# Kernel tuning notes

Hardware: AMD Instinct MI355X
Metric: run time of the kernel (lower is better)

## Reference

```python
import jax, jax.numpy as jnp
import numpy as np

N_NODES = 50000
N_EDGES = 800000
IN_F = 64
OUT_F = 64
HEADS = 4
ALPHA = 0.2  # LeakyReLU negative slope


def setup_inputs() -> dict:
    key = jax.random.key(0)
    k1, k2, k3, k4, k5, k6 = jax.random.split(key, 6)
    x = jax.random.normal(k1, (N_NODES, IN_F), dtype=jnp.float32)
    src = jax.random.randint(k2, (N_EDGES,), 0, N_NODES)
    dst = jax.random.randint(k3, (N_EDGES,), 0, N_NODES)
    edge_index = jnp.stack([src, dst]).astype(jnp.int64)
    # learned params: per-head projection + attention vectors (GAT)
    W = jax.random.normal(k4, (HEADS, IN_F, OUT_F), dtype=jnp.float32) * 0.1
    a_src = jax.random.normal(k5, (HEADS, OUT_F), dtype=jnp.float32) * 0.1
    a_dst = jax.random.normal(k6, (HEADS, OUT_F), dtype=jnp.float32) * 0.1
    return {"x": x, "edge_index": edge_index, "W": W, "a_src": a_src, "a_dst": a_dst}


def reference(x, edge_index, W, a_src, a_dst):
    N = x.shape[0]
    src, dst = edge_index[0], edge_index[1]
    # per-head projection: [N, H, O]
    h = jnp.einsum('nf,hfo->nho', x, W)
    # node-level attention halves: [N, H]
    s_src = jnp.einsum('nho,ho->nh', h, a_src)
    s_dst = jnp.einsum('nho,ho->nh', h, a_dst)
    # edge logits with LeakyReLU: [E, H]
    e = jax.nn.leaky_relu(s_src[src] + s_dst[dst], negative_slope=ALPHA)
    # segment softmax over incoming edges of each destination node
    e_max = jax.ops.segment_max(e, dst, num_segments=N)  # [N, H]
    e_exp = jnp.exp(e - e_max[dst])
    denom = jax.ops.segment_sum(e_exp, dst, num_segments=N)  # [N, H]
    attn = e_exp / (denom[dst] + 1e-16)  # [E, H]
    # weighted scatter-aggregation: [N, H, O]
    msg = h[src] * attn[:, :, None]
    out = jax.ops.segment_sum(msg, dst, num_segments=N)
    # average_head=False -> concatenate heads; no bias, no activation
    return out.reshape(N, HEADS * OUT_F)
```

## Files before the change

kernel.cpp:

```cpp
#include <hip/hip_runtime.h>

#define HEADS 4
#define OUTF 64
#define INF 64
#define CAP 48

typedef __attribute__((ext_vector_type(8))) short bf16x8;
typedef __attribute__((ext_vector_type(4))) float f32x4;

__device__ __forceinline__ ushort f2bf(float f) {
    const unsigned u = __float_as_uint(f);
    return (ushort)((u + 0x7fffu + ((u >> 16) & 1u)) >> 16);
}

__global__ __launch_bounds__(256) void prep_kernel(
    const float* __restrict__ W, const float* __restrict__ a_src,
    const float* __restrict__ a_dst, float* __restrict__ va_s, float* __restrict__ va_d,
    ushort* __restrict__ W_packed, const int* __restrict__ ei, int* __restrict__ flag,
    int* __restrict__ deg, int N)
{
    const int t = threadIdx.x;
    for (int i = blockIdx.x * 256 + t; i < N; i += gridDim.x * 256) deg[i] = 0;

    if (blockIdx.x == 8) {
        if (t == 0) {
            int all0 = 1;
            #pragma unroll
            for (int k = 1; k < 64; k += 2) all0 &= (ei[k] == 0);
            *flag = all0;
        }
        const int h = t >> 6;
        const float* Wr = W + (size_t)t * 64;
        const float* as = a_src + h * 64;
        const float* ad = a_dst + h * 64;
        float s = 0.f, d = 0.f;
        #pragma unroll
        for (int o = 0; o < 64; ++o) {
            const float wv = Wr[o];
            s = fmaf(wv, as[o], s);
            d = fmaf(wv, ad[o], d);
        }
        va_s[t] = s;
        va_d[t] = d;
        return;
    }
    const int idx  = blockIdx.x * 256 + t;
    const int tile = idx >> 7;
    const int st   = (idx >> 6) & 1;
    const int l    = idx & 63;
    const int o_g  = tile * 16 + (l & 15);
    const int hh   = o_g >> 6;
    const int oo   = o_g & 63;
    const int k0   = st * 32 + (l >> 4) * 8;
    ushort v[8];
    #pragma unroll
    for (int i = 0; i < 8; ++i)
        v[i] = f2bf(W[(size_t)hh * 4096 + (size_t)(k0 + i) * 64 + oo]);
    uint4 u;
    u.x = v[0] | ((unsigned)v[1] << 16);
    u.y = v[2] | ((unsigned)v[3] << 16);
    u.z = v[4] | ((unsigned)v[5] << 16);
    u.w = v[6] | ((unsigned)v[7] << 16);
    *reinterpret_cast<uint4*>(W_packed + (size_t)idx * 8) = u;
}

__global__ __launch_bounds__(256) void s_fill_kernel(
    const float* __restrict__ x, const float* __restrict__ va_s,
    const float* __restrict__ va_d, float* __restrict__ ssrc,
    float* __restrict__ sdst, ushort* __restrict__ x_bf,
    const int* __restrict__ ei, const int* __restrict__ flag,
    int* __restrict__ deg, ushort* __restrict__ csr_src, int N, int E)
{
    const int nid = blockIdx.x * 256 + threadIdx.x;
    if (nid < N) {
        const float* xr = x + (size_t)nid * 64;
        float rs[4] = {0.f, 0.f, 0.f, 0.f};
        float rd[4] = {0.f, 0.f, 0.f, 0.f};
        #pragma unroll
        for (int f4 = 0; f4 < 16; ++f4) {
            const float4 xv = *reinterpret_cast<const float4*>(xr + 4 * f4);
            uint2 xb;
            xb.x = f2bf(xv.x) | ((unsigned)f2bf(xv.y) << 16);
            xb.y = f2bf(xv.z) | ((unsigned)f2bf(xv.w) << 16);
            *reinterpret_cast<uint2*>(x_bf + (size_t)nid * 64 + 4 * f4) = xb;
            #pragma unroll
            for (int h = 0; h < 4; ++h) {
                const float4 s4 = *reinterpret_cast<const float4*>(va_s + h * 64 + 4 * f4);
                const float4 d4 = *reinterpret_cast<const float4*>(va_d + h * 64 + 4 * f4);
                rs[h] = fmaf(xv.x, s4.x, fmaf(xv.y, s4.y, fmaf(xv.z, s4.z, fmaf(xv.w, s4.w, rs[h]))));
                rd[h] = fmaf(xv.x, d4.x, fmaf(xv.y, d4.y, fmaf(xv.z, d4.z, fmaf(xv.w, d4.w, rd[h]))));
            }
        }
        *reinterpret_cast<float4*>(ssrc + (size_t)nid * 4) = make_float4(rs[0], rs[1], rs[2], rs[3]);
        *reinterpret_cast<float4*>(sdst + (size_t)nid * 4) = make_float4(rd[0], rd[1], rd[2], rd[3]);
    }

    const int i64v  = *flag;
    const int g     = blockIdx.x & 7;
    const int lo    = g * (N >> 3);
    const int hi    = (g == 7) ? N : lo + (N >> 3);
    const int tgl   = (blockIdx.x >> 3) * 256 + threadIdx.x;
    const int gstep = (gridDim.x >> 3) * 256;

    if (i64v) {
        for (int e = tgl * 4; e + 4 <= E; e += gstep * 4) {
            const int4 d01 = *reinterpret_cast<const int4*>(ei + 2 * (size_t)E + 2 * (size_t)e);
            const int4 d23 = *reinterpret_cast<const int4*>(ei + 2 * (size_t)E + 2 * (size_t)e + 4);
            const int dd[4] = {d01.x, d01.z, d23.x, d23.z};
            bool any = false;
            #pragma unroll
            for (int k = 0; k < 4; ++k) any |= (dd[k] >= lo && dd[k] < hi);
            if (!any) continue;
            const int4 s01 = *reinterpret_cast<const int4*>(ei + 2 * (size_t)e);
            const int4 s23 = *reinterpret_cast<const int4*>(ei + 2 * (size_t)e + 4);
            const int ss[4] = {s01.x, s01.z, s23.x, s23.z};
            #pragma unroll
            for (int k = 0; k < 4; ++k) {
                if (dd[k] >= lo && dd[k] < hi) {
                    const int pos = atomicAdd(&deg[dd[k]], 1);
                    if (pos < CAP) csr_src[(size_t)dd[k] * CAP + pos] = (ushort)ss[k];
                }
            }
        }
    } else {
        for (int e = tgl * 4; e + 4 <= E; e += gstep * 4) {
            const int4 dv = *reinterpret_cast<const int4*>(ei + (size_t)E + e);
            const int dd[4] = {dv.x, dv.y, dv.z, dv.w};
            bool any = false;
            #pragma unroll
            for (int k = 0; k < 4; ++k) any |= (dd[k] >= lo && dd[k] < hi);
            if (!any) continue;
            const int4 sv = *reinterpret_cast<const int4*>(ei + e);
            const int ss[4] = {sv.x, sv.y, sv.z, sv.w};
            #pragma unroll
            for (int k = 0; k < 4; ++k) {
                if (dd[k] >= lo && dd[k] < hi) {
                    const int pos = atomicAdd(&deg[dd[k]], 1);
                    if (pos < CAP) csr_src[(size_t)dd[k] * CAP + pos] = (ushort)ss[k];
                }
            }
        }
    }
    if (blockIdx.x < 8 && threadIdx.x == 0) {
        for (int i = E & ~3; i < E; ++i) {
            int src, dst;
            if (i64v) { src = ei[2 * (size_t)i]; dst = ei[2 * ((size_t)E + i)]; }
            else      { src = ei[i];             dst = ei[(size_t)E + i]; }
            if (dst >= lo && dst < hi) {
                const int pos = atomicAdd(&deg[dst], 1);
                if (pos < CAP) csr_src[(size_t)dst * CAP + pos] = (ushort)src;
            }
        }
    }
}

#define ACCUM(XV, SS) do { \
    float e0 = (SS).x + sd4.x, e1 = (SS).y + sd4.y, e2 = (SS).z + sd4.z, e3 = (SS).w + sd4.w; \
    e0 = e0 >= 0.f ? e0 : 0.2f * e0; \
    e1 = e1 >= 0.f ? e1 : 0.2f * e1; \
    e2 = e2 >= 0.f ? e2 : 0.2f * e2; \
    e3 = e3 >= 0.f ? e3 : 0.2f * e3; \
    const float w0 = __expf(e0), w1 = __expf(e1), w2 = __expf(e2), w3 = __expf(e3); \
    const float f0 = __uint_as_float((XV).x << 16); \
    const float f1 = __uint_as_float((XV).x & 0xffff0000u); \
    const float f2 = __uint_as_float((XV).y << 16); \
    const float f3 = __uint_as_float((XV).y & 0xffff0000u); \
    A00 = fmaf(w0, f0, A00); A01 = fmaf(w0, f1, A01); A02 = fmaf(w0, f2, A02); A03 = fmaf(w0, f3, A03); \
    A10 = fmaf(w1, f0, A10); A11 = fmaf(w1, f1, A11); A12 = fmaf(w1, f2, A12); A13 = fmaf(w1, f3, A13); \
    A20 = fmaf(w2, f0, A20); A21 = fmaf(w2, f1, A21); A22 = fmaf(w2, f2, A22); A23 = fmaf(w2, f3, A23); \
    A30 = fmaf(w3, f0, A30); A31 = fmaf(w3, f1, A31); A32 = fmaf(w3, f2, A32); A33 = fmaf(w3, f3, A33); \
    ws0 += w0; ws1 += w1; ws2 += w2; ws3 += w3; \
} while (0)

#define CHUNK(SV, CNT) do { \
    int j = 0; \
    for (; j + 2 <= (CNT); j += 2) { \
        const int sA = __shfl((SV), g0 + j); \
        const int sB = __shfl((SV), g0 + j + 1); \
        const uint2 xA = *reinterpret_cast<const uint2*>(x_bf + ((size_t)sA << 6) + (l4 << 2)); \
        const uint2 xB = *reinterpret_cast<const uint2*>(x_bf + ((size_t)sB << 6) + (l4 << 2)); \
        const float4 pA = *reinterpret_cast<const float4*>(ssrc + 4 * (size_t)sA); \
        const float4 pB = *reinterpret_cast<const float4*>(ssrc + 4 * (size_t)sB); \
        ACCUM(xA, pA); \
        ACCUM(xB, pB); \
    } \
    if (j < (CNT)) { \
        const int sA = __shfl((SV), g0 + j); \
        const uint2 xA = *reinterpret_cast<const uint2*>(x_bf + ((size_t)sA << 6) + (l4 << 2)); \
        const float4 pA = *reinterpret_cast<const float4*>(ssrc + 4 * (size_t)sA); \
        ACCUM(xA, pA); \
    } \
} while (0)

__global__ __launch_bounds__(256) void gather_out(
    const int* __restrict__ deg, const ushort* __restrict__ csr_src,
    const ushort* __restrict__ x_bf, const float* __restrict__ ssrc,
    const float* __restrict__ sdst, const ushort* __restrict__ W_packed,
    float* __restrict__ out, int N)
{
    __shared__ ushort agg_lds[16][264];

    const int tid  = threadIdx.x;
    const int lane = tid & 63;
    const int l4   = lane & 15;
    const int g0   = lane & 48;
    const int wv   = tid >> 6;
    const int nl   = wv * 4 + (lane >> 4);
    const int n    = blockIdx.x * 16 + nl;
    const size_t base = (size_t)n * CAP;
    const int d    = min(deg[n], CAP);

    const int sv0 = (int)csr_src[base + l4];
    const int sv1 = (int)csr_src[base + 16 + l4];
    const int sv2 = (int)csr_src[base + 32 + l4];

    const float4 sd4 = *reinterpret_cast<const float4*>(sdst + (size_t)n * 4);

    float A00 = 0.f, A01 = 0.f, A02 = 0.f, A03 = 0.f;
    float A10 = 0.f, A11 = 0.f, A12 = 0.f, A13 = 0.f;
    float A20 = 0.f, A21 = 0.f, A22 = 0.f, A23 = 0.f;
    float A30 = 0.f, A31 = 0.f, A32 = 0.f, A33 = 0.f;
    float ws0 = 0.f, ws1 = 0.f, ws2 = 0.f, ws3 = 0.f;

    const int c0 = min(d, 16);
    const int c1 = min(max(d - 16, 0), 16);
    const int c2 = min(max(d - 32, 0), 16);
    CHUNK(sv0, c0);
    CHUNK(sv1, c1);
    CHUNK(sv2, c2);

    ushort* ap = &agg_lds[nl][l4 << 2];
    const float i0 = 1.f / (ws0 + 1e-16f);
    const float i1 = 1.f / (ws1 + 1e-16f);
    const float i2 = 1.f / (ws2 + 1e-16f);
    const float i3 = 1.f / (ws3 + 1e-16f);
    uint2 o;
    o.x = f2bf(A00 * i0) | ((unsigned)f2bf(A01 * i0) << 16);
    o.y = f2bf(A02 * i0) | ((unsigned)f2bf(A03 * i0) << 16);
    *reinterpret_cast<uint2*>(ap) = o;
    o.x = f2bf(A10 * i1) | ((unsigned)f2bf(A11 * i1) << 16);
    o.y = f2bf(A12 * i1) | ((unsigned)f2bf(A13 * i1) << 16);
    *reinterpret_cast<uint2*>(ap + 64) = o;
    o.x = f2bf(A20 * i2) | ((unsigned)f2bf(A21 * i2) << 16);
    o.y = f2bf(A22 * i2) | ((unsigned)f2bf(A23 * i2) << 16);
    *reinterpret_cast<uint2*>(ap + 128) = o;
    o.x = f2bf(A30 * i3) | ((unsigned)f2bf(A31 * i3) << 16);
    o.y = f2bf(A32 * i3) | ((unsigned)f2bf(A33 * i3) << 16);
    *reinterpret_cast<uint2*>(ap + 192) = o;

    __syncthreads();

    const int r    = lane & 15;
    const int kb   = (lane >> 4) * 8;
    const int hoff = wv * 64;
    const bf16x8 a0 = *reinterpret_cast<const bf16x8*>(&agg_lds[r][hoff + kb]);
    const bf16x8 a1 = *reinterpret_cast<const bf16x8*>(&agg_lds[r][hoff + 32 + kb]);

    const int drow = (lane >> 4) * 4;
    const int nb0  = blockIdx.x * 16;
    #pragma unroll
    for (int tt = 0; tt < 4; ++tt) {
        const int tile = wv * 4 + tt;
        const bf16x8 b0 = *reinterpret_cast<const bf16x8*>(W_packed + ((size_t)(tile * 2 + 0) * 64 + lane) * 8);
        const bf16x8 b1 = *reinterpret_cast<const bf16x8*>(W_packed + ((size_t)(tile * 2 + 1) * 64 + lane) * 8);
        f32x4 acc = {0.f, 0.f, 0.f, 0.f};
        acc = __builtin_amdgcn_mfma_f32_16x16x32_bf16(a0, b0, acc, 0, 0, 0);
        acc = __builtin_amdgcn_mfma_f32_16x16x32_bf16(a1, b1, acc, 0, 0, 0);
        const int col = tile * 16 + r;
        #pragma unroll
        for (int i = 0; i < 4; ++i)
            out[(size_t)(nb0 + drow + i) * 256 + col] = acc[i];
    }
}

extern "C" void kernel_launch(void* const* d_in, const int* in_sizes, int n_in,
                              void* d_out, int out_size, void* d_ws, size_t ws_size,
                              hipStream_t stream) {
    const float* x     = (const float*)d_in[0];
    const int*   ei    = (const int*)d_in[1];
    const float* W     = (const float*)d_in[2];
    const float* a_src = (const float*)d_in[3];
    const float* a_dst = (const float*)d_in[4];
    float*       out   = (float*)d_out;

    const int N = in_sizes[0] / INF;
    const int E = in_sizes[1] / 2;

    ushort* x_bf     = (ushort*)d_ws;
    ushort* W_packed = x_bf + (size_t)N * 64;
    float* ssrc      = (float*)(W_packed + 16384);
    float* sdst      = ssrc + (size_t)N * 4;
    float* va_s      = sdst + (size_t)N * 4;
    float* va_d      = va_s + 256;
    int*   deg       = (int*)(va_d + 256);
    ushort* csr_src  = (ushort*)(deg + N);
    int*   flag      = (int*)(csr_src + (size_t)N * CAP);

    const int nblk_fill = 1024;

    prep_kernel<<<9, 256, 0, stream>>>(W, a_src, a_dst, va_s, va_d, W_packed, ei, flag, deg, N);
    s_fill_kernel<<<nblk_fill, 256, 0, stream>>>(x, va_s, va_d, ssrc, sdst, x_bf, ei, flag, deg, csr_src, N, E);
    gather_out<<<N / 16, 256, 0, stream>>>(deg, csr_src, x_bf, ssrc, sdst, W_packed, out, N);
}
```

Before: 88.98 us.

## Precompute per-edge bf16 attention weights during CSR fill, split node-score kernel

Splits the node-score/bf16-conversion work from the CSR fill into a separate kernel so the fill can read finished scores. The fill now computes each edge's LeakyReLU and exp2 (log2e folded into the attention vectors) and stores packed bf16 weights next to the CSR source index. The gather then reads these weights instead of doing a random ssrc lookup and exp per edge. The cost is an extra launch and serialization between score and fill, extra random ssrc/sdst reads plus weight writes in the fill, and bf16 rounding of the softmax weights. The max-subtraction is still skipped, as before.

```diff
diff --git a/kernel.cpp b/kernel.cpp
--- a/kernel.cpp
+++ b/kernel.cpp
@@ -40,8 +40,8 @@
             s = fmaf(wv, as[o], s);
             d = fmaf(wv, ad[o], d);
         }
-        va_s[t] = s;
-        va_d[t] = d;
+        va_s[t] = s * 1.44269504f;
+        va_d[t] = d * 1.44269504f;
         return;
     }
     const int idx  = blockIdx.x * 256 + t;
@@ -64,37 +64,41 @@
     *reinterpret_cast<uint4*>(W_packed + (size_t)idx * 8) = u;
 }
 
-__global__ __launch_bounds__(256) void s_fill_kernel(
+__global__ __launch_bounds__(256) void s_node_kernel(
     const float* __restrict__ x, const float* __restrict__ va_s,
     const float* __restrict__ va_d, float* __restrict__ ssrc,
-    float* __restrict__ sdst, ushort* __restrict__ x_bf,
-    const int* __restrict__ ei, const int* __restrict__ flag,
-    int* __restrict__ deg, ushort* __restrict__ csr_src, int N, int E)
+    float* __restrict__ sdst, ushort* __restrict__ x_bf, int N)
 {
     const int nid = blockIdx.x * 256 + threadIdx.x;
-    if (nid < N) {
-        const float* xr = x + (size_t)nid * 64;
-        float rs[4] = {0.f, 0.f, 0.f, 0.f};
-        float rd[4] = {0.f, 0.f, 0.f, 0.f};
-        #pragma unroll
-        for (int f4 = 0; f4 < 16; ++f4) {
-            const float4 xv = *reinterpret_cast<const float4*>(xr + 4 * f4);
-            uint2 xb;
-            xb.x = f2bf(xv.x) | ((unsigned)f2bf(xv.y) << 16);
-            xb.y = f2bf(xv.z) | ((unsigned)f2bf(xv.w) << 16);
-            *reinterpret_cast<uint2*>(x_bf + (size_t)nid * 64 + 4 * f4) = xb;
-            #pragma unroll
-            for (int h = 0; h < 4; ++h) {
-                const float4 s4 = *reinterpret_cast<const float4*>(va_s + h * 64 + 4 * f4);
-                const float4 d4 = *reinterpret_cast<const float4*>(va_d + h * 64 + 4 * f4);
-                rs[h] = fmaf(xv.x, s4.x, fmaf(xv.y, s4.y, fmaf(xv.z, s4.z, fmaf(xv.w, s4.w, rs[h]))));
-                rd[h] = fmaf(xv.x, d4.x, fmaf(xv.y, d4.y, fmaf(xv.z, d4.z, fmaf(xv.w, d4.w, rd[h]))));
-            }
-        }
-        *reinterpret_cast<float4*>(ssrc + (size_t)nid * 4) = make_float4(rs[0], rs[1], rs[2], rs[3]);
-        *reinterpret_cast<float4*>(sdst + (size_t)nid * 4) = make_float4(rd[0], rd[1], rd[2], rd[3]);
-    }
-
+    if (nid >= N) return;
+    const float* xr = x + (size_t)nid * 64;
+    float rs[4] = {0.f, 0.f, 0.f, 0.f};
+    float rd[4] = {0.f, 0.f, 0.f, 0.f};
+    #pragma unroll
+    for (int f4 = 0; f4 < 16; ++f4) {
+        const float4 xv = *reinterpret_cast<const float4*>(xr + 4 * f4);
+        uint2 xb;
+        xb.x = f2bf(xv.x) | ((unsigned)f2bf(xv.y) << 16);
+        xb.y = f2bf(xv.z) | ((unsigned)f2bf(xv.w) << 16);
+        *reinterpret_cast<uint2*>(x_bf + (size_t)nid * 64 + 4 * f4) = xb;
+        #pragma unroll
+        for (int h = 0; h < 4; ++h) {
+            const float4 s4 = *reinterpret_cast<const float4*>(va_s + h * 64 + 4 * f4);
+            const float4 d4 = *reinterpret_cast<const float4*>(va_d + h * 64 + 4 * f4);
+            rs[h] = fmaf(xv.x, s4.x, fmaf(xv.y, s4.y, fmaf(xv.z, s4.z, fmaf(xv.w, s4.w, rs[h]))));
+            rd[h] = fmaf(xv.x, d4.x, fmaf(xv.y, d4.y, fmaf(xv.z, d4.z, fmaf(xv.w, d4.w, rd[h]))));
+        }
+    }
+    *reinterpret_cast<float4*>(ssrc + (size_t)nid * 4) = make_float4(rs[0], rs[1], rs[2], rs[3]);
+    *reinterpret_cast<float4*>(sdst + (size_t)nid * 4) = make_float4(rd[0], rd[1], rd[2], rd[3]);
+}
+
+__global__ __launch_bounds__(256) void fill_kernel(
+    const int* __restrict__ ei, const int* __restrict__ flag,
+    const float* __restrict__ ssrc, const float* __restrict__ sdst,
+    int* __restrict__ deg, ushort* __restrict__ csr_src,
+    ushort* __restrict__ csr_w, int N, int E)
+{
     const int i64v  = *flag;
     const int g     = blockIdx.x & 7;
     const int lo    = g * (N >> 3);
@@ -102,41 +106,46 @@
     const int tgl   = (blockIdx.x >> 3) * 256 + threadIdx.x;
     const int gstep = (gridDim.x >> 3) * 256;
 
-    if (i64v) {
-        for (int e = tgl * 4; e + 4 <= E; e += gstep * 4) {
+    for (int e = tgl * 4; e + 4 <= E; e += gstep * 4) {
+        int dd[4], ss[4];
+        if (i64v) {
             const int4 d01 = *reinterpret_cast<const int4*>(ei + 2 * (size_t)E + 2 * (size_t)e);
             const int4 d23 = *reinterpret_cast<const int4*>(ei + 2 * (size_t)E + 2 * (size_t)e + 4);
-            const int dd[4] = {d01.x, d01.z, d23.x, d23.z};
-            bool any = false;
-            #pragma unroll
-            for (int k = 0; k < 4; ++k) any |= (dd[k] >= lo && dd[k] < hi);
-            if (!any) continue;
+            dd[0] = d01.x; dd[1] = d01.z; dd[2] = d23.x; dd[3] = d23.z;
+        } else {
+            const int4 dv = *reinterpret_cast<const int4*>(ei + (size_t)E + e);
+            dd[0] = dv.x; dd[1] = dv.y; dd[2] = dv.z; dd[3] = dv.w;
+        }
+        bool any = false;
+        #pragma unroll
+        for (int k = 0; k < 4; ++k) any |= (dd[k] >= lo && dd[k] < hi);
+        if (!any) continue;
+        if (i64v) {
             const int4 s01 = *reinterpret_cast<const int4*>(ei + 2 * (size_t)e);
             const int4 s23 = *reinterpret_cast<const int4*>(ei + 2 * (size_t)e + 4);
-            const int ss[4] = {s01.x, s01.z, s23.x, s23.z};
-            #pragma unroll
-            for (int k = 0; k < 4; ++k) {
-                if (dd[k] >= lo && dd[k] < hi) {
-                    const int pos = atomicAdd(&deg[dd[k]], 1);
-                    if (pos < CAP) csr_src[(size_t)dd[k] * CAP + pos] = (ushort)ss[k];
-                }
-            }
-        }
-    } else {
-        for (int e = tgl * 4; e + 4 <= E; e += gstep * 4) {
-            const int4 dv = *reinterpret_cast<const int4*>(ei + (size_t)E + e);
-            const int dd[4] = {dv.x, dv.y, dv.z, dv.w};
-            bool any = false;
-            #pragma unroll
-            for (int k = 0; k < 4; ++k) any |= (dd[k] >= lo && dd[k] < hi);
-            if (!any) continue;
+            ss[0] = s01.x; ss[1] = s01.z; ss[2] = s23.x; ss[3] = s23.z;
+        } else {
             const int4 sv = *reinterpret_cast<const int4*>(ei + e);
-            const int ss[4] = {sv.x, sv.y, sv.z, sv.w};
-            #pragma unroll
-            for (int k = 0; k < 4; ++k) {
-                if (dd[k] >= lo && dd[k] < hi) {
-                    const int pos = atomicAdd(&deg[dd[k]], 1);
-                    if (pos < CAP) csr_src[(size_t)dd[k] * CAP + pos] = (ushort)ss[k];
+            ss[0] = sv.x; ss[1] = sv.y; ss[2] = sv.z; ss[3] = sv.w;
+        }
+        #pragma unroll
+        for (int k = 0; k < 4; ++k) {
+            if (dd[k] >= lo && dd[k] < hi) {
+                const int pos = atomicAdd(&deg[dd[k]], 1);
+                if (pos < CAP) {
+                    const size_t slot = (size_t)dd[k] * CAP + pos;
+                    csr_src[slot] = (ushort)ss[k];
+                    const float4 s4 = *reinterpret_cast<const float4*>(ssrc + 4 * (size_t)ss[k]);
+                    const float4 d4 = *reinterpret_cast<const float4*>(sdst + 4 * (size_t)dd[k]);
+                    float w0 = s4.x + d4.x, w1 = s4.y + d4.y, w2 = s4.z + d4.z, w3 = s4.w + d4.w;
+                    w0 = fmaxf(w0, 0.2f * w0);
+                    w1 = fmaxf(w1, 0.2f * w1);
+                    w2 = fmaxf(w2, 0.2f * w2);
+                    w3 = fmaxf(w3, 0.2f * w3);
+                    uint2 wp;
+                    wp.x = f2bf(exp2f(w0)) | ((unsigned)f2bf(exp2f(w1)) << 16);
+                    wp.y = f2bf(exp2f(w2)) | ((unsigned)f2bf(exp2f(w3)) << 16);
+                    *reinterpret_cast<uint2*>(csr_w + slot * 4) = wp;
                 }
             }
         }
@@ -148,19 +157,31 @@
             else      { src = ei[i];             dst = ei[(size_t)E + i]; }
             if (dst >= lo && dst < hi) {
                 const int pos = atomicAdd(&deg[dst], 1);
-                if (pos < CAP) csr_src[(size_t)dst * CAP + pos] = (ushort)src;
+                if (pos < CAP) {
+                    const size_t slot = (size_t)dst * CAP + pos;
+                    csr_src[slot] = (ushort)src;
+                    const float4 s4 = *reinterpret_cast<const float4*>(ssrc + 4 * (size_t)src);
+                    const float4 d4 = *reinterpret_cast<const float4*>(sdst + 4 * (size_t)dst);
+                    float w0 = s4.x + d4.x, w1 = s4.y + d4.y, w2 = s4.z + d4.z, w3 = s4.w + d4.w;
+                    w0 = fmaxf(w0, 0.2f * w0);
+                    w1 = fmaxf(w1, 0.2f * w1);
+                    w2 = fmaxf(w2, 0.2f * w2);
+                    w3 = fmaxf(w3, 0.2f * w3);
+                    uint2 wp;
+                    wp.x = f2bf(exp2f(w0)) | ((unsigned)f2bf(exp2f(w1)) << 16);
+                    wp.y = f2bf(exp2f(w2)) | ((unsigned)f2bf(exp2f(w3)) << 16);
+                    *reinterpret_cast<uint2*>(csr_w + slot * 4) = wp;
+                }
             }
         }
     }
 }
 
-#define ACCUM(XV, SS) do { \
-    float e0 = (SS).x + sd4.x, e1 = (SS).y + sd4.y, e2 = (SS).z + sd4.z, e3 = (SS).w + sd4.w; \
-    e0 = e0 >= 0.f ? e0 : 0.2f * e0; \
-    e1 = e1 >= 0.f ? e1 : 0.2f * e1; \
-    e2 = e2 >= 0.f ? e2 : 0.2f * e2; \
-    e3 = e3 >= 0.f ? e3 : 0.2f * e3; \
-    const float w0 = __expf(e0), w1 = __expf(e1), w2 = __expf(e2), w3 = __expf(e3); \
+#define ACCW(XV, WV) do { \
+    const float w0 = __uint_as_float((WV).x << 16); \
+    const float w1 = __uint_as_float((WV).x & 0xffff0000u); \
+    const float w2 = __uint_as_float((WV).y << 16); \
+    const float w3 = __uint_as_float((WV).y & 0xffff0000u); \
     const float f0 = __uint_as_float((XV).x << 16); \
     const float f1 = __uint_as_float((XV).x & 0xffff0000u); \
     const float f2 = __uint_as_float((XV).y << 16); \
@@ -172,31 +193,30 @@
     ws0 += w0; ws1 += w1; ws2 += w2; ws3 += w3; \
 } while (0)
 
-#define CHUNK(SV, CNT) do { \
+#define CHUNKW(SV, OFF, CNT) do { \
     int j = 0; \
     for (; j + 2 <= (CNT); j += 2) { \
         const int sA = __shfl((SV), g0 + j); \
         const int sB = __shfl((SV), g0 + j + 1); \
         const uint2 xA = *reinterpret_cast<const uint2*>(x_bf + ((size_t)sA << 6) + (l4 << 2)); \
         const uint2 xB = *reinterpret_cast<const uint2*>(x_bf + ((size_t)sB << 6) + (l4 << 2)); \
-        const float4 pA = *reinterpret_cast<const float4*>(ssrc + 4 * (size_t)sA); \
-        const float4 pB = *reinterpret_cast<const float4*>(ssrc + 4 * (size_t)sB); \
-        ACCUM(xA, pA); \
-        ACCUM(xB, pB); \
+        const uint2 wA = *reinterpret_cast<const uint2*>(csr_w + (base + (OFF) + j) * 4); \
+        const uint2 wB = *reinterpret_cast<const uint2*>(csr_w + (base + (OFF) + j + 1) * 4); \
+        ACCW(xA, wA); \
+        ACCW(xB, wB); \
     } \
     if (j < (CNT)) { \
         const int sA = __shfl((SV), g0 + j); \
         const uint2 xA = *reinterpret_cast<const uint2*>(x_bf + ((size_t)sA << 6) + (l4 << 2)); \
-        const float4 pA = *reinterpret_cast<const float4*>(ssrc + 4 * (size_t)sA); \
-        ACCUM(xA, pA); \
+        const uint2 wA = *reinterpret_cast<const uint2*>(csr_w + (base + (OFF) + j) * 4); \
+        ACCW(xA, wA); \
     } \
 } while (0)
 
 __global__ __launch_bounds__(256) void gather_out(
     const int* __restrict__ deg, const ushort* __restrict__ csr_src,
-    const ushort* __restrict__ x_bf, const float* __restrict__ ssrc,
-    const float* __restrict__ sdst, const ushort* __restrict__ W_packed,
-    float* __restrict__ out, int N)
+    const ushort* __restrict__ csr_w, const ushort* __restrict__ x_bf,
+    const ushort* __restrict__ W_packed, float* __restrict__ out, int N)
 {
     __shared__ ushort agg_lds[16][264];
 
@@ -214,8 +234,6 @@
     const int sv1 = (int)csr_src[base + 16 + l4];
     const int sv2 = (int)csr_src[base + 32 + l4];
 
-    const float4 sd4 = *reinterpret_cast<const float4*>(sdst + (size_t)n * 4);
-
     float A00 = 0.f, A01 = 0.f, A02 = 0.f, A03 = 0.f;
     float A10 = 0.f, A11 = 0.f, A12 = 0.f, A13 = 0.f;
     float A20 = 0.f, A21 = 0.f, A22 = 0.f, A23 = 0.f;
@@ -225,9 +243,9 @@
     const int c0 = min(d, 16);
     const int c1 = min(max(d - 16, 0), 16);
     const int c2 = min(max(d - 32, 0), 16);
-    CHUNK(sv0, c0);
-    CHUNK(sv1, c1);
-    CHUNK(sv2, c2);
+    CHUNKW(sv0, 0, c0);
+    CHUNKW(sv1, 16, c1);
+    CHUNKW(sv2, 32, c2);
 
     ushort* ap = &agg_lds[nl][l4 << 2];
     const float i0 = 1.f / (ws0 + 1e-16f);
@@ -294,11 +312,11 @@
     float* va_d      = va_s + 256;
     int*   deg       = (int*)(va_d + 256);
     ushort* csr_src  = (ushort*)(deg + N);
-    int*   flag      = (int*)(csr_src + (size_t)N * CAP);
-
-    const int nblk_fill = 1024;
+    ushort* csr_w    = csr_src + (size_t)N * CAP;
+    int*   flag      = (int*)(csr_w + (size_t)N * CAP * 4);
 
     prep_kernel<<<9, 256, 0, stream>>>(W, a_src, a_dst, va_s, va_d, W_packed, ei, flag, deg, N);
-    s_fill_kernel<<<nblk_fill, 256, 0, stream>>>(x, va_s, va_d, ssrc, sdst, x_bf, ei, flag, deg, csr_src, N, E);
-    gather_out<<<N / 16, 256, 0, stream>>>(deg, csr_src, x_bf, ssrc, sdst, W_packed, out, N);
-}
+    s_node_kernel<<<(N + 255) / 256, 256, 0, stream>>>(x, va_s, va_d, ssrc, sdst, x_bf, N);
+    fill_kernel<<<1024, 256, 0, stream>>>(ei, flag, ssrc, sdst, deg, csr_src, csr_w, N, E);
+    gather_out<<<N / 16, 256, 0, stream>>>(deg, csr_src, csr_w, x_bf, W_packed, out, N);
+}
```

Result: slower. 98.26 us (+10.4%).
